# Kernel tuning notes

Measured on AMD Instinct MI355X. Metric: run time of the kernel, lower is better.

## Reference

```python
import jax, jax.numpy as jnp
import numpy as np

B, C, L = 4, 64, 4096
RED = 4          # reduction -> q/k channels = C // RED = 16
N_HASHES = 4
HASH_BUCKETS = min(L // 4, 32)  # = 32, matches torch code
EPS = 1e-5


def _conv1x1(x, W, b):
    # x: [B, Cin, L], W: [Cout, Cin], b: [Cout]
    return jnp.einsum('bcl,oc->bol', x, W) + b[None, :, None]


def setup_inputs() -> dict:
    key = jax.random.key(0)
    ks = jax.random.split(key, 12)
    Cq = C // RED
    x = jax.random.normal(ks[0], (B, C, L), dtype=jnp.float32)
    hash_idx = jax.random.randint(ks[1], (B, N_HASHES, L), 0, HASH_BUCKETS, dtype=jnp.int32)
    sC = 1.0 / np.sqrt(C)
    Wq = jax.random.normal(ks[2], (Cq, C), dtype=jnp.float32) * sC
    bq = jax.random.normal(ks[3], (Cq,), dtype=jnp.float32) * 0.01
    Wk = jax.random.normal(ks[4], (Cq, C), dtype=jnp.float32) * sC
    bk = jax.random.normal(ks[5], (Cq,), dtype=jnp.float32) * 0.01
    Wv = jax.random.normal(ks[6], (C, C), dtype=jnp.float32) * sC
    bv = jax.random.normal(ks[7], (C,), dtype=jnp.float32) * 0.01
    Wo = jax.random.normal(ks[8], (C, C), dtype=jnp.float32) * sC
    bo = jax.random.normal(ks[9], (C,), dtype=jnp.float32) * 0.01
    gamma = jax.random.normal(ks[10], (1,), dtype=jnp.float32)  # nonzero so attn path matters
    bn_w = jnp.ones((C,), dtype=jnp.float32)
    bn_b = jnp.zeros((C,), dtype=jnp.float32)
    return dict(x=x, hash_idx=hash_idx, Wq=Wq, bq=bq, Wk=Wk, bk=bk,
                Wv=Wv, bv=bv, Wo=Wo, bo=bo, gamma=gamma, bn_w=bn_w, bn_b=bn_b)


def reference(x, hash_idx, Wq, bq, Wk, bk, Wv, bv, Wo, bo, gamma, bn_w, bn_b):
    # 1x1 conv projections
    q = _conv1x1(x, Wq, bq)   # [B, C/RED, L]
    k = _conv1x1(x, Wk, bk)   # [B, C/RED, L]
    v = _conv1x1(x, Wv, bv)   # [B, C, L]

    qT = q.transpose(0, 2, 1)  # [B, L, Cq]
    kT = k.transpose(0, 2, 1)
    vT = v.transpose(0, 2, 1)  # [B, L, C]

    # raw scores are hash-independent; only the bucket mask changes per hash
    scores = jnp.einsum('bic,bjc->bij', qT, kT)  # [B, L, L], no sqrt(d) scaling (matches torch)

    n_hashes = hash_idx.shape[1]
    acc = jnp.zeros_like(vT)
    for h in range(n_hashes):  # small fixed loop
        idx = hash_idx[:, h, :]                       # [B, L]
        mask = idx[:, :, None] == idx[:, None, :]     # same-bucket mask [B, L, L]
        s = jnp.where(mask, scores, -1e9)
        attn = jax.nn.softmax(s, axis=-1)             # within-bucket softmax (diag always valid)
        acc = acc + jnp.einsum('bij,bjc->bic', attn, vT)
    attn_out = (acc / n_hashes).transpose(0, 2, 1)    # [B, C, L], averaged over hashes

    out = _conv1x1(attn_out, Wo, bo)
    out = gamma * out + x                             # residual with learned scalar

    # BatchNorm1d, training mode: biased batch stats over (B, L) per channel
    mean = out.mean(axis=(0, 2), keepdims=True)
    var = out.var(axis=(0, 2), keepdims=True)
    out = (out - mean) * jax.lax.rsqrt(var + EPS)
    out = out * bn_w[None, :, None] + bn_b[None, :, None]
    return out
```

## Files before the change

kernel.cpp:

```cpp
#include <hip/hip_runtime.h>
#include <math.h>

#define Bn 4
#define Cn 64
#define Ln 4096
#define CQ 16
#define NH 4
#define NB 32
#define EPSV 1e-5f

#define MAXS 384
#define CH2 64
#define KSTR 20
#define VSTR 64

#define QSZ   (Bn*Ln*CQ)
#define VSZ   (Bn*Ln*Cn)
#define ACCSZ (Bn*Ln*Cn)
#define NBH   (Bn*NH)

#define OFF_K   QSZ
#define OFF_V   (2*QSZ)
#define OFF_ACC (2*QSZ + VSZ)

#define LOG2E 1.44269504088896f

__global__ __launch_bounds__(256) void proj_kernel(
        const float* __restrict__ x,
        const float* __restrict__ Wq, const float* __restrict__ bq,
        const float* __restrict__ Wk, const float* __restrict__ bk,
        const float* __restrict__ Wv, const float* __restrict__ bv,
        float* __restrict__ q, float* __restrict__ k, float* __restrict__ v) {
    __shared__ float sWt[Cn*32];
    __shared__ float sb[32];
    int tid = threadIdx.x;
    int third = blockIdx.x % 3;
    int pg    = blockIdx.x / 3;
    int rbase = third * 32;
    for (int idx = tid; idx < Cn*32; idx += 256) {
        int rr = idx & 31, c = idx >> 5;
        int r = rbase + rr;
        float w;
        if (r < 16)      w = Wq[r*Cn + c];
        else if (r < 32) w = Wk[(r-16)*Cn + c];
        else             w = Wv[(r-32)*Cn + c];
        sWt[c*32 + rr] = w;
    }
    if (tid < 32) {
        int r = rbase + tid;
        sb[tid] = (r < 16) ? bq[r] : (r < 32 ? bk[r-16] : bv[r-32]);
    }
    __syncthreads();
    int p = tid & 63, og = tid >> 6;
    int gp = pg * 64 + p;
    int b = gp >> 12, l = gp & (Ln - 1);
    const float* xp = &x[b*Cn*Ln + l];
    int rr0 = og * 8;
    float val[8];
    #pragma unroll
    for (int i = 0; i < 8; i++) val[i] = sb[rr0 + i];
    #pragma unroll
    for (int c0 = 0; c0 < Cn; c0 += 8) {
        float xv[8];
        #pragma unroll
        for (int i = 0; i < 8; i++) xv[i] = xp[(c0 + i)*Ln];
        #pragma unroll
        for (int i = 0; i < 8; i++) {
            const float* wrow = &sWt[(c0 + i)*32 + rr0];
            #pragma unroll
            for (int j = 0; j < 8; j++) val[j] = fmaf(wrow[j], xv[i], val[j]);
        }
    }
    int f = third*8 + og*2;
    float4 t0 = make_float4(val[0], val[1], val[2], val[3]);
    float4 t1 = make_float4(val[4], val[5], val[6], val[7]);
    float4* q4 = (float4*)&q[gp*CQ];
    float4* k4 = (float4*)&k[gp*CQ];
    float4* v4 = (float4*)&v[gp*Cn];
    if (f < 4)      { q4[f]   = t0; q4[f+1] = t1; }
    else if (f < 8) { k4[f-4] = t0; k4[f-3] = t1; }
    else            { v4[f-8] = t0; v4[f-7] = t1; }
}

template<int NS, int MODE>
__device__ __forceinline__ void attn_pass(
        int qbase, int S, int b, int h, int tid, int rem,
        const int* list, float* ks, float* vs,
        const float* __restrict__ q, const float* __restrict__ k,
        const float* __restrict__ v, float* __restrict__ acc) {
    int qd = tid >> 2, c4 = tid & 3;
    float4 qr[NS][4];
    float4 o[NS][4];
    float lsum[NS];
    int qi[NS], iqr[NS];
    #pragma unroll
    for (int s = 0; s < NS; s++) {
        qi[s] = qbase + 64*s + qd;
        iqr[s] = 0;
        lsum[s] = 0.f;
        #pragma unroll
        for (int i = 0; i < 4; i++) o[s][i] = make_float4(0.f,0.f,0.f,0.f);
        if (qi[s] < S) {
            iqr[s] = list[qi[s]];
            const float4* qp = (const float4*)&q[(b*Ln + iqr[s])*CQ];
            #pragma unroll
            for (int i = 0; i < 4; i++) {
                float4 t = qp[i];
                t.x*=LOG2E; t.y*=LOG2E; t.z*=LOG2E; t.w*=LOG2E;
                qr[s][i] = t;
            }
        } else {
            #pragma unroll
            for (int i = 0; i < 4; i++) qr[s][i] = make_float4(0.f,0.f,0.f,0.f);
        }
    }
    for (int cc = 0; cc < S; cc += CH2) {
        int nk = min(CH2, S - cc);
        __syncthreads();
        {
            int jj = tid >> 2, cf = tid & 3;
            if (jj < nk) {
                const float4* kp = (const float4*)&k[(b*Ln + list[cc+jj])*CQ];
                *(float4*)&ks[jj*KSTR + cf*4] = kp[cf];
            }
        }
        #pragma unroll
        for (int uu = 0; uu < 4; uu++) {
            int idx = uu*256 + tid;
            int jj = idx >> 4, cf = idx & 15;
            if (jj < nk) {
                const float4* vp = (const float4*)&v[(b*Ln + list[cc+jj])*Cn];
                *(float4*)&vs[jj*VSTR + cf*4] = vp[cf];
            }
        }
        __syncthreads();
        if (rem > 0) {
            for (int j = 0; j < nk; j++) {
                const float4* kr = (const float4*)&ks[j*KSTR];
                float4 k0 = kr[0], k1 = kr[1], k2 = kr[2], k3 = kr[3];
                const float4* vp4 = (const float4*)&vs[j*VSTR + c4*16];
                float4 v0 = vp4[0], v1 = vp4[1], v2 = vp4[2], v3 = vp4[3];
                #pragma unroll
                for (int s = 0; s < NS; s++) {
                    float s0 = qr[s][0].x*k0.x + qr[s][0].y*k0.y + qr[s][0].z*k0.z + qr[s][0].w*k0.w;
                    float s1 = qr[s][1].x*k1.x + qr[s][1].y*k1.y + qr[s][1].z*k1.z + qr[s][1].w*k1.w;
                    float s2 = qr[s][2].x*k2.x + qr[s][2].y*k2.y + qr[s][2].z*k2.z + qr[s][2].w*k2.w;
                    float s3 = qr[s][3].x*k3.x + qr[s][3].y*k3.y + qr[s][3].z*k3.z + qr[s][3].w*k3.w;
                    float pw = __builtin_amdgcn_exp2f((s0 + s1) + (s2 + s3));
                    lsum[s] += pw;
                    o[s][0].x = fmaf(pw, v0.x, o[s][0].x); o[s][0].y = fmaf(pw, v0.y, o[s][0].y);
                    o[s][0].z = fmaf(pw, v0.z, o[s][0].z); o[s][0].w = fmaf(pw, v0.w, o[s][0].w);
                    o[s][1].x = fmaf(pw, v1.x, o[s][1].x); o[s][1].y = fmaf(pw, v1.y, o[s][1].y);
                    o[s][1].z = fmaf(pw, v1.z, o[s][1].z); o[s][1].w = fmaf(pw, v1.w, o[s][1].w);
                    o[s][2].x = fmaf(pw, v2.x, o[s][2].x); o[s][2].y = fmaf(pw, v2.y, o[s][2].y);
                    o[s][2].z = fmaf(pw, v2.z, o[s][2].z); o[s][2].w = fmaf(pw, v2.w, o[s][2].w);
                    o[s][3].x = fmaf(pw, v3.x, o[s][3].x); o[s][3].y = fmaf(pw, v3.y, o[s][3].y);
                    o[s][3].z = fmaf(pw, v3.z, o[s][3].z); o[s][3].w = fmaf(pw, v3.w, o[s][3].w);
                }
            }
        }
    }
    #pragma unroll
    for (int s = 0; s < NS; s++) {
        if (qi[s] < S) {
            float inv = 1.f / lsum[s];
            #pragma unroll
            for (int i = 0; i < 4; i++) {
                o[s][i].x*=inv; o[s][i].y*=inv; o[s][i].z*=inv; o[s][i].w*=inv;
            }
            if (MODE == 1) {
                float4* ap = (float4*)&acc[((size_t)h*Bn*Ln + b*Ln + iqr[s])*Cn + c4*16];
                ap[0]=o[s][0]; ap[1]=o[s][1]; ap[2]=o[s][2]; ap[3]=o[s][3];
            } else {
                float* ap = &acc[(b*Ln + iqr[s])*Cn + c4*16];
                #pragma unroll
                for (int i = 0; i < 4; i++) {
                    atomicAdd(&ap[4*i+0], (&o[s][i].x)[0]);
                    atomicAdd(&ap[4*i+1], (&o[s][i].x)[1]);
                    atomicAdd(&ap[4*i+2], (&o[s][i].x)[2]);
                    atomicAdd(&ap[4*i+3], (&o[s][i].x)[3]);
                }
            }
        }
    }
}

template<int MODE>
__global__ __launch_bounds__(256, 2) void attn_kernel(
        const float* __restrict__ q, const float* __restrict__ k,
        const float* __restrict__ v, const int* __restrict__ hidx,
        float* __restrict__ acc) {
    __shared__ int list[MAXS];
    __shared__ float ks[CH2*KSTR];
    __shared__ float vs[CH2*VSTR];
    __shared__ int wtot[4];
    int blk = blockIdx.x;
    int u  = blk & (NB-1);
    int bh = blk >> 5;
    int b  = bh >> 2;
    int h  = bh & 3;
    int tid = threadIdx.x;

    const int4* hp4 = (const int4*)(&hidx[bh*Ln] + tid*16);
    int hv[16];
    #pragma unroll
    for (int t = 0; t < 4; t++) {
        int4 tmp = hp4[t];
        hv[t*4+0]=tmp.x; hv[t*4+1]=tmp.y; hv[t*4+2]=tmp.z; hv[t*4+3]=tmp.w;
    }
    int myCnt = 0;
    #pragma unroll
    for (int t = 0; t < 16; t++) myCnt += (hv[t] == u);
    int lane = tid & 63, wv = tid >> 6;
    int pre = myCnt;
    #pragma unroll
    for (int d = 1; d < 64; d <<= 1) {
        int t = __shfl_up(pre, d, 64);
        if (lane >= d) pre += t;
    }
    if (lane == 63) wtot[wv] = pre;
    __syncthreads();
    int base = 0;
    #pragma unroll
    for (int w = 0; w < 4; w++) base += (w < wv) ? wtot[w] : 0;
    int Sall = wtot[0] + wtot[1] + wtot[2] + wtot[3];
    int S = min(Sall, MAXS);
    int excl = base + pre - myCnt;
    #pragma unroll
    for (int t = 0; t < 16; t++) {
        if (hv[t] == u) {
            if (excl < MAXS) list[excl] = tid*16 + t;
            excl++;
        }
    }
    __syncthreads();

    int wq0 = (tid >> 6) << 4;
    for (int qbase = 0; qbase < S; qbase += 192) {
        int rem = S - qbase - wq0;
        if (rem > 128)     attn_pass<3,MODE>(qbase,S,b,h,tid,rem,list,ks,vs,q,k,v,acc);
        else if (rem > 64) attn_pass<2,MODE>(qbase,S,b,h,tid,rem,list,ks,vs,q,k,v,acc);
        else               attn_pass<1,MODE>(qbase,S,b,h,tid,rem,list,ks,vs,q,k,v,acc);
    }
}

template<int MODE>
__global__ __launch_bounds__(256) void outconv_kernel(
        const float* __restrict__ acc, const float* __restrict__ Wo,
        const float* __restrict__ bo, const float* __restrict__ gamma,
        const float* __restrict__ x, float* __restrict__ y) {
    __shared__ float sWt[Cn*32];
    __shared__ float sb[32];
    int tid = threadIdx.x;
    int half = blockIdx.x & 1;
    int pg   = blockIdx.x >> 1;
    for (int idx = tid; idx < Cn*32; idx += 256) {
        int oo = idx & 31, c = idx >> 5;
        sWt[c*32 + oo] = Wo[(half*32 + oo)*Cn + c];
    }
    if (tid < 32) sb[tid] = bo[half*32 + tid];
    __syncthreads();
    float g = gamma[0];
    int p = tid & 63, og = tid >> 6;
    int gp = pg * 64 + p;
    int b = gp >> 12, l = gp & (Ln - 1);
    int oo0 = og * 8;
    float val[8];
    #pragma unroll
    for (int i = 0; i < 8; i++) val[i] = sb[oo0 + i];
    const float4* ap0 = (const float4*)&acc[(size_t)gp*Cn];
    #pragma unroll
    for (int c4 = 0; c4 < 16; c4++) {
        float4 t = ap0[c4];
        if (MODE == 1) {
            float4 t1 = ap0[(size_t)ACCSZ/4   + c4];
            float4 t2 = ap0[(size_t)ACCSZ/4*2 + c4];
            float4 t3 = ap0[(size_t)ACCSZ/4*3 + c4];
            t.x += t1.x + t2.x + t3.x; t.y += t1.y + t2.y + t3.y;
            t.z += t1.z + t2.z + t3.z; t.w += t1.w + t2.w + t3.w;
        }
        float a0 = t.x*0.25f, a1 = t.y*0.25f, a2 = t.z*0.25f, a3 = t.w*0.25f;
        const float* w0 = &sWt[(c4*4+0)*32 + oo0];
        const float* w1 = &sWt[(c4*4+1)*32 + oo0];
        const float* w2 = &sWt[(c4*4+2)*32 + oo0];
        const float* w3 = &sWt[(c4*4+3)*32 + oo0];
        #pragma unroll
        for (int i = 0; i < 8; i++) {
            val[i] = fmaf(w0[i], a0, val[i]);
            val[i] = fmaf(w1[i], a1, val[i]);
            val[i] = fmaf(w2[i], a2, val[i]);
            val[i] = fmaf(w3[i], a3, val[i]);
        }
    }
    #pragma unroll
    for (int i = 0; i < 8; i++) {
        int o = half*32 + oo0 + i;
        float yv = fmaf(g, val[i], x[(b*Cn + o)*Ln + l]);
        y[(b*Cn + o)*Ln + l] = yv;
    }
}

__global__ __launch_bounds__(256) void stats_kernel(
        const float* __restrict__ y, float* __restrict__ ssum, float* __restrict__ ssq) {
    int c = blockIdx.x >> 2;
    int part = blockIdx.x & 3;
    int tid = threadIdx.x;
    const float4* yp = (const float4*)&y[(part*Cn + c)*Ln];
    float s = 0.f, s2 = 0.f;
    #pragma unroll
    for (int i = 0; i < 4; i++) {
        float4 t = yp[i*256 + tid];
        s  += t.x + t.y + t.z + t.w;
        s2 += t.x*t.x + t.y*t.y + t.z*t.z + t.w*t.w;
    }
    #pragma unroll
    for (int w = 1; w < 64; w <<= 1) {
        s  += __shfl_xor(s,  w, 64);
        s2 += __shfl_xor(s2, w, 64);
    }
    __shared__ float rs[4], rs2[4];
    int wv = tid >> 6;
    if ((tid & 63) == 0) { rs[wv] = s; rs2[wv] = s2; }
    __syncthreads();
    if (tid == 0) {
        atomicAdd(&ssum[c], rs[0]+rs[1]+rs[2]+rs[3]);
        atomicAdd(&ssq[c],  rs2[0]+rs2[1]+rs2[2]+rs2[3]);
    }
}

__global__ __launch_bounds__(256) void norm_kernel(
        const float* __restrict__ y,
        const float* __restrict__ ssum, const float* __restrict__ ssq,
        const float* __restrict__ bnw, const float* __restrict__ bnb,
        float* __restrict__ out) {
    int idx = blockIdx.x * 256 + threadIdx.x;
    int flat = idx * 4;
    int c = (flat / Ln) & 63;
    const float n = (float)(Bn*Ln);
    float mu = ssum[c] / n;
    float var = ssq[c] / n - mu*mu;
    float is = rsqrtf(var + EPSV);
    float w = is * bnw[c];
    float bb = bnb[c] - mu * w;
    float4 t = ((const float4*)y)[idx];
    float4 r;
    r.x = t.x*w + bb; r.y = t.y*w + bb; r.z = t.z*w + bb; r.w = t.w*w + bb;
    ((float4*)out)[idx] = r;
}

extern "C" void kernel_launch(void* const* d_in, const int* in_sizes, int n_in,
                              void* d_out, int out_size, void* d_ws, size_t ws_size,
                              hipStream_t stream) {
    const float* x    = (const float*)d_in[0];
    const int*   hidx = (const int*)  d_in[1];
    const float* Wq   = (const float*)d_in[2];
    const float* bq   = (const float*)d_in[3];
    const float* Wk   = (const float*)d_in[4];
    const float* bk   = (const float*)d_in[5];
    const float* Wv   = (const float*)d_in[6];
    const float* bv   = (const float*)d_in[7];
    const float* Wo   = (const float*)d_in[8];
    const float* bo   = (const float*)d_in[9];
    const float* gam  = (const float*)d_in[10];
    const float* bnw  = (const float*)d_in[11];
    const float* bnb  = (const float*)d_in[12];
    float* out = (float*)d_out;

    float* ws  = (float*)d_ws;
    float* q   = ws;
    float* k   = ws + OFF_K;
    float* v   = ws + OFF_V;
    float* acc = ws + OFF_ACC;
    float* y   = ws;

    const size_t bigNeed = ((size_t)OFF_ACC + 4*(size_t)ACCSZ + 2*Cn) * sizeof(float);
    bool big = ws_size >= bigNeed;
    float* ssum = acc + (big ? 4*(size_t)ACCSZ : (size_t)ACCSZ);
    float* ssq  = ssum + Cn;

    hipMemsetAsync(ssum, 0, 2*Cn*sizeof(float), stream);

    proj_kernel<<<Bn*Ln/64*3, 256, 0, stream>>>(x, Wq, bq, Wk, bk, Wv, bv, q, k, v);
    if (big) {
        attn_kernel<1><<<NBH*NB, 256, 0, stream>>>(q, k, v, hidx, acc);
        outconv_kernel<1><<<Bn*Ln/64*2, 256, 0, stream>>>(acc, Wo, bo, gam, x, y);
    } else {
        hipMemsetAsync(acc, 0, (size_t)ACCSZ*sizeof(float), stream);
        attn_kernel<0><<<NBH*NB, 256, 0, stream>>>(q, k, v, hidx, acc);
        outconv_kernel<0><<<Bn*Ln/64*2, 256, 0, stream>>>(acc, Wo, bo, gam, x, y);
    }
    stats_kernel<<<Cn*4, 256, 0, stream>>>(y, ssum, ssq);
    norm_kernel<<<Bn*Cn*Ln/4/256, 256, 0, stream>>>(y, ssum, ssq, bnw, bnb, out);
}
```

Before: 182.2 us.

## Restage outconv via shared-memory transposed tile; replace stats atomics with partials

```diff
diff --git a/kernel.cpp b/kernel.cpp
--- a/kernel.cpp
+++ b/kernel.cpp
@@ -102,7 +102,7 @@
         for (int i = 0; i < 4; i++) o[s][i] = make_float4(0.f,0.f,0.f,0.f);
         if (qi[s] < S) {
             iqr[s] = list[qi[s]];
-            const float4* qp = (const float4*)&q[(b*Ln + iqr[s])*CQ];
+            const float4* qp = (const float4*)&q[((size_t)b*Ln + iqr[s])*CQ];
             #pragma unroll
             for (int i = 0; i < 4; i++) {
                 float4 t = qp[i];
@@ -120,7 +120,7 @@
         {
             int jj = tid >> 2, cf = tid & 3;
             if (jj < nk) {
-                const float4* kp = (const float4*)&k[(b*Ln + list[cc+jj])*CQ];
+                const float4* kp = (const float4*)&k[((size_t)b*Ln + list[cc+jj])*CQ];
                 *(float4*)&ks[jj*KSTR + cf*4] = kp[cf];
             }
         }
@@ -129,7 +129,7 @@
             int idx = uu*256 + tid;
             int jj = idx >> 4, cf = idx & 15;
             if (jj < nk) {
-                const float4* vp = (const float4*)&v[(b*Ln + list[cc+jj])*Cn];
+                const float4* vp = (const float4*)&v[((size_t)b*Ln + list[cc+jj])*Cn];
                 *(float4*)&vs[jj*VSTR + cf*4] = vp[cf];
             }
         }
@@ -172,7 +172,7 @@
                 float4* ap = (float4*)&acc[((size_t)h*Bn*Ln + b*Ln + iqr[s])*Cn + c4*16];
                 ap[0]=o[s][0]; ap[1]=o[s][1]; ap[2]=o[s][2]; ap[3]=o[s][3];
             } else {
-                float* ap = &acc[(b*Ln + iqr[s])*Cn + c4*16];
+                float* ap = &acc[((size_t)b*Ln + iqr[s])*Cn + c4*16];
                 #pragma unroll
                 for (int i = 0; i < 4; i++) {
                     atomicAdd(&ap[4*i+0], (&o[s][i].x)[0]);
@@ -249,59 +249,60 @@
         const float* __restrict__ acc, const float* __restrict__ Wo,
         const float* __restrict__ bo, const float* __restrict__ gamma,
         const float* __restrict__ x, float* __restrict__ y) {
-    __shared__ float sWt[Cn*32];
-    __shared__ float sb[32];
+    __shared__ float sWt[Cn*Cn];
+    __shared__ float sA[Cn*33];
+    __shared__ float sb[Cn];
     int tid = threadIdx.x;
-    int half = blockIdx.x & 1;
-    int pg   = blockIdx.x >> 1;
-    for (int idx = tid; idx < Cn*32; idx += 256) {
-        int oo = idx & 31, c = idx >> 5;
-        sWt[c*32 + oo] = Wo[(half*32 + oo)*Cn + c];
-    }
-    if (tid < 32) sb[tid] = bo[half*32 + tid];
-    __syncthreads();
-    float g = gamma[0];
-    int p = tid & 63, og = tid >> 6;
-    int gp = pg * 64 + p;
-    int b = gp >> 12, l = gp & (Ln - 1);
-    int oo0 = og * 8;
-    float val[8];
-    #pragma unroll
-    for (int i = 0; i < 8; i++) val[i] = sb[oo0 + i];
-    const float4* ap0 = (const float4*)&acc[(size_t)gp*Cn];
-    #pragma unroll
-    for (int c4 = 0; c4 < 16; c4++) {
-        float4 t = ap0[c4];
+    int pg = blockIdx.x;
+    for (int idx = tid; idx < Cn*Cn; idx += 256) {
+        int o = idx & 63, c = idx >> 6;
+        sWt[c*Cn + o] = Wo[o*Cn + c];
+    }
+    if (tid < Cn) sb[tid] = bo[tid];
+    const float4* a4 = (const float4*)&acc[(size_t)pg*32*Cn];
+    #pragma unroll
+    for (int r = 0; r < 2; r++) {
+        int idx = r*256 + tid;
+        int p = idx >> 4, c0 = (idx & 15) * 4;
+        float4 t = a4[idx];
         if (MODE == 1) {
-            float4 t1 = ap0[(size_t)ACCSZ/4   + c4];
-            float4 t2 = ap0[(size_t)ACCSZ/4*2 + c4];
-            float4 t3 = ap0[(size_t)ACCSZ/4*3 + c4];
+            float4 t1 = a4[(size_t)ACCSZ/4   + idx];
+            float4 t2 = a4[(size_t)ACCSZ/4*2 + idx];
+            float4 t3 = a4[(size_t)ACCSZ/4*3 + idx];
             t.x += t1.x + t2.x + t3.x; t.y += t1.y + t2.y + t3.y;
             t.z += t1.z + t2.z + t3.z; t.w += t1.w + t2.w + t3.w;
         }
-        float a0 = t.x*0.25f, a1 = t.y*0.25f, a2 = t.z*0.25f, a3 = t.w*0.25f;
-        const float* w0 = &sWt[(c4*4+0)*32 + oo0];
-        const float* w1 = &sWt[(c4*4+1)*32 + oo0];
-        const float* w2 = &sWt[(c4*4+2)*32 + oo0];
-        const float* w3 = &sWt[(c4*4+3)*32 + oo0];
-        #pragma unroll
-        for (int i = 0; i < 8; i++) {
-            val[i] = fmaf(w0[i], a0, val[i]);
-            val[i] = fmaf(w1[i], a1, val[i]);
-            val[i] = fmaf(w2[i], a2, val[i]);
-            val[i] = fmaf(w3[i], a3, val[i]);
-        }
+        sA[(c0+0)*33 + p] = t.x*0.25f;
+        sA[(c0+1)*33 + p] = t.y*0.25f;
+        sA[(c0+2)*33 + p] = t.z*0.25f;
+        sA[(c0+3)*33 + p] = t.w*0.25f;
+    }
+    __syncthreads();
+    float g = gamma[0];
+    int p = tid & 31, og = tid >> 5;
+    int gp = pg * 32 + p;
+    int b = gp >> 12, l = gp & (Ln - 1);
+    int o0 = og * 8;
+    float val[8];
+    #pragma unroll
+    for (int i = 0; i < 8; i++) val[i] = sb[o0 + i];
+    #pragma unroll
+    for (int c = 0; c < Cn; c++) {
+        float av = sA[c*33 + p];
+        const float* wrow = &sWt[c*Cn + o0];
+        #pragma unroll
+        for (int i = 0; i < 8; i++) val[i] = fmaf(wrow[i], av, val[i]);
     }
     #pragma unroll
     for (int i = 0; i < 8; i++) {
-        int o = half*32 + oo0 + i;
+        int o = o0 + i;
         float yv = fmaf(g, val[i], x[(b*Cn + o)*Ln + l]);
         y[(b*Cn + o)*Ln + l] = yv;
     }
 }
 
 __global__ __launch_bounds__(256) void stats_kernel(
-        const float* __restrict__ y, float* __restrict__ ssum, float* __restrict__ ssq) {
+        const float* __restrict__ y, float* __restrict__ ssumP, float* __restrict__ ssqP) {
     int c = blockIdx.x >> 2;
     int part = blockIdx.x & 3;
     int tid = threadIdx.x;
@@ -323,22 +324,25 @@
     if ((tid & 63) == 0) { rs[wv] = s; rs2[wv] = s2; }
     __syncthreads();
     if (tid == 0) {
-        atomicAdd(&ssum[c], rs[0]+rs[1]+rs[2]+rs[3]);
-        atomicAdd(&ssq[c],  rs2[0]+rs2[1]+rs2[2]+rs2[3]);
+        ssumP[blockIdx.x] = rs[0]+rs[1]+rs[2]+rs[3];
+        ssqP[blockIdx.x]  = rs2[0]+rs2[1]+rs2[2]+rs2[3];
     }
 }
 
 __global__ __launch_bounds__(256) void norm_kernel(
         const float* __restrict__ y,
-        const float* __restrict__ ssum, const float* __restrict__ ssq,
+        const float* __restrict__ ssumP, const float* __restrict__ ssqP,
         const float* __restrict__ bnw, const float* __restrict__ bnb,
         float* __restrict__ out) {
     int idx = blockIdx.x * 256 + threadIdx.x;
     int flat = idx * 4;
     int c = (flat / Ln) & 63;
+    float s = 0.f, s2 = 0.f;
+    #pragma unroll
+    for (int hh = 0; hh < 4; hh++) { s += ssumP[c*4+hh]; s2 += ssqP[c*4+hh]; }
     const float n = (float)(Bn*Ln);
-    float mu = ssum[c] / n;
-    float var = ssq[c] / n - mu*mu;
+    float mu = s / n;
+    float var = s2 / n - mu*mu;
     float is = rsqrtf(var + EPSV);
     float w = is * bnw[c];
     float bb = bnb[c] - mu * w;
@@ -373,22 +377,20 @@
     float* acc = ws + OFF_ACC;
     float* y   = ws;
 
-    const size_t bigNeed = ((size_t)OFF_ACC + 4*(size_t)ACCSZ + 2*Cn) * sizeof(float);
+    const size_t bigNeed = ((size_t)OFF_ACC + 4*(size_t)ACCSZ + 512) * sizeof(float);
     bool big = ws_size >= bigNeed;
-    float* ssum = acc + (big ? 4*(size_t)ACCSZ : (size_t)ACCSZ);
-    float* ssq  = ssum + Cn;
-
-    hipMemsetAsync(ssum, 0, 2*Cn*sizeof(float), stream);
+    float* ssumP = acc + (big ? 4*(size_t)ACCSZ : (size_t)ACCSZ);
+    float* ssqP  = ssumP + 256;
 
     proj_kernel<<<Bn*Ln/64*3, 256, 0, stream>>>(x, Wq, bq, Wk, bk, Wv, bv, q, k, v);
     if (big) {
         attn_kernel<1><<<NBH*NB, 256, 0, stream>>>(q, k, v, hidx, acc);
-        outconv_kernel<1><<<Bn*Ln/64*2, 256, 0, stream>>>(acc, Wo, bo, gam, x, y);
+        outconv_kernel<1><<<Bn*Ln/32, 256, 0, stream>>>(acc, Wo, bo, gam, x, y);
     } else {
         hipMemsetAsync(acc, 0, (size_t)ACCSZ*sizeof(float), stream);
         attn_kernel<0><<<NBH*NB, 256, 0, stream>>>(q, k, v, hidx, acc);
-        outconv_kernel<0><<<Bn*Ln/64*2, 256, 0, stream>>>(acc, Wo, bo, gam, x, y);
-    }
-    stats_kernel<<<Cn*4, 256, 0, stream>>>(y, ssum, ssq);
-    norm_kernel<<<Bn*Cn*Ln/4/256, 256, 0, stream>>>(y, ssum, ssq, bnw, bnb, out);
-}
+        outconv_kernel<0><<<Bn*Ln/32, 256, 0, stream>>>(acc, Wo, bo, gam, x, y);
+    }
+    stats_kernel<<<Cn*4, 256, 0, stream>>>(y, ssumP, ssqP);
+    norm_kernel<<<Bn*Cn*Ln/4/256, 256, 0, stream>>>(y, ssumP, ssqP, bnw, bnb, out);
+}
```

After: 169.3 us. 7.1% less time.
